# Kernel optimization log

Measured on AMD Instinct MI355X. Metric: run time of the kernel, lower is better.

The kernel has to match this reference:

```python
import jax, jax.numpy as jnp
import numpy as np

K = 3  # deformable kernel size -> K*K = 9 sampling points
EPS = 1e-5


def _bilinear_sample(img, py, px):
    """Bilinear sample img (B,H,W,C) at float pixel coords py,px (B,H,W), zero padding."""
    B, H, W, C = img.shape
    y0f = jnp.floor(py); x0f = jnp.floor(px)
    wy = py - y0f; wx = px - x0f
    y0 = y0f.astype(jnp.int32); x0 = x0f.astype(jnp.int32)
    bidx = jnp.arange(B)[:, None, None]
    out = jnp.zeros(img.shape, img.dtype)
    corners = ((0, 0, (1 - wy) * (1 - wx)), (0, 1, (1 - wy) * wx),
               (1, 0, wy * (1 - wx)), (1, 1, wy * wx))
    for dy, dx, w in corners:
        yy = y0 + dy; xx = x0 + dx
        valid = ((yy >= 0) & (yy < H) & (xx >= 0) & (xx < W)).astype(img.dtype)
        yc = jnp.clip(yy, 0, H - 1); xc = jnp.clip(xx, 0, W - 1)
        out = out + (w * valid)[..., None] * img[bidx, yc, xc]
    return out


def setup_inputs() -> dict:
    key = jax.random.key(0)
    ks = jax.random.split(key, 8)
    B, C, H, W = 8, 256, 64, 64
    return {
        "x1": jax.random.normal(ks[0], (B, C, H, W), jnp.float32),
        "x2": jax.random.normal(ks[1], (B, C, H // 2, W // 2), jnp.float32),
        "dw_w": jax.random.normal(ks[2], (3, 3, 1, C), jnp.float32) * 0.05,
        "dw_b": jnp.zeros((C,), jnp.float32),
        "ln_g": jnp.ones((C,), jnp.float32),
        "ln_b": jnp.zeros((C,), jnp.float32),
        "off_w": jax.random.normal(ks[3], (C, 2 * K * K), jnp.float32) * 0.01,
        "off_b": jnp.zeros((2 * K * K,), jnp.float32),
        "mask_w": jax.random.normal(ks[4], (C, K * K), jnp.float32) * 0.02,
        "mask_b": jnp.zeros((K * K,), jnp.float32),
        "in_w": jax.random.normal(ks[5], (C, C), jnp.float32) * 0.02,
        "in_b": jnp.zeros((C,), jnp.float32),
        "out_w": jax.random.normal(ks[6], (C, C), jnp.float32) * 0.02,
        "out_b": jnp.zeros((C,), jnp.float32),
        "bn_g": jnp.ones((C,), jnp.float32),
        "bn_b": jnp.zeros((C,), jnp.float32),
        "bn_mean": jnp.zeros((C,), jnp.float32),
        "bn_var": jnp.ones((C,), jnp.float32),
    }


def _forward(x1, x2, dw_w, dw_b, ln_g, ln_b, off_w, off_b, mask_w, mask_b,
             in_w, in_b, out_w, out_b, bn_g, bn_b, bn_mean, bn_var):
    B, C, H, W = x1.shape
    # interpolate x2 -> (H,W), bilinear (half-pixel centers, align_corners=False)
    x2r = jax.image.resize(x2, (B, C, H, W), method="linear")
    x21, x22 = jnp.split(x2r, 2, axis=0)
    diff = jnp.abs(x21 - x22)
    guide = jnp.concatenate([diff, diff], axis=0)  # repeat(2,1,1,1)

    v = jnp.transpose(x1, (0, 2, 3, 1))      # (B,H,W,C) values
    f = jnp.transpose(guide, (0, 2, 3, 1))   # (B,H,W,C) guidance

    # DCNv3 input projection
    x_proj = v @ in_w + in_b

    # depthwise 3x3 conv + LayerNorm + GELU on guidance
    feat = jax.lax.conv_general_dilated(
        f, dw_w, (1, 1), "SAME",
        dimension_numbers=("NHWC", "HWIO", "NHWC"),
        feature_group_count=C) + dw_b
    mu = jnp.mean(feat, axis=-1, keepdims=True)
    var = jnp.var(feat, axis=-1, keepdims=True)
    feat = (feat - mu) * jax.lax.rsqrt(var + EPS) * ln_g + ln_b
    feat = jax.nn.gelu(feat)

    offset = (feat @ off_w + off_b).reshape(B, H, W, K * K, 2)  # (..., (dx,dy))
    mask = jax.nn.softmax(feat @ mask_w + mask_b, axis=-1)       # (B,H,W,9)

    base_y = jnp.arange(H, dtype=x1.dtype)[:, None]
    base_x = jnp.arange(W, dtype=x1.dtype)[None, :]
    acc = jnp.zeros((B, H, W, C), x1.dtype)
    for k in range(K * K):
        ky = k // K - 1
        kx = k % K - 1
        py = base_y + ky + offset[..., k, 1]
        px = base_x + kx + offset[..., k, 0]
        acc = acc + mask[..., k:k + 1] * _bilinear_sample(x_proj, py, px)

    y = acc @ out_w + out_b                  # output projection
    y = jnp.transpose(y, (0, 3, 1, 2))       # back to NCHW

    # BatchNorm (inference stats) + ReLU + residual
    scale = bn_g * jax.lax.rsqrt(bn_var + EPS)
    y = y * scale[None, :, None, None] + (bn_b - bn_mean * scale)[None, :, None, None]
    return jax.nn.relu(y) + x1


def reference(x1, x2, dw_w, dw_b, ln_g, ln_b, off_w, off_b, mask_w, mask_b,
              in_w, in_b, out_w, out_b, bn_g, bn_b, bn_mean, bn_var):
    return _forward(x1, x2, dw_w, dw_b, ln_g, ln_b, off_w, off_b, mask_w, mask_b,
                    in_w, in_b, out_w, out_b, bn_g, bn_b, bn_mean, bn_var)
```

## Files before the change

### kernel.cpp

```cpp
#include <hip/hip_runtime.h>
#include <math.h>

#define BB 8
#define CC 256
#define HH 64
#define WW 64
#define H2 32
#define W2 32
#define NPIX (BB*HH*WW)
#define EPSV 1e-5f

typedef unsigned short ushortT;
using short8  = __attribute__((ext_vector_type(8))) short;
using floatx4 = __attribute__((ext_vector_type(4))) float;

__device__ inline float b2f(ushortT u) {
    unsigned int x = ((unsigned int)u) << 16;
    float f; __builtin_memcpy(&f, &x, 4); return f;
}
__device__ inline ushortT f2b(float f) {
    unsigned int x; __builtin_memcpy(&x, &f, 4);
    unsigned int r = x + 0x7fffu + ((x >> 16) & 1u);
    return (ushortT)(r >> 16);
}

__global__ __launch_bounds__(256) void k1_both(const float* __restrict__ x2,
        const float* __restrict__ x1, const float* __restrict__ in_w,
        const float* __restrict__ in_b, const float* __restrict__ out_w,
        const float* __restrict__ off_w, const float* __restrict__ mask_w,
        ushortT* __restrict__ guide, ushortT* __restrict__ x1t,
        ushortT* __restrict__ Bf, float* __restrict__ bwout,
        ushortT* __restrict__ Whf) {
    __shared__ __align__(16) float Xs[2 * 64 * 2 * 33];
    __shared__ __align__(16) ushortT tile[64 * 66];
    int blk0 = blockIdx.x;
    int t = threadIdx.x;

    if (blk0 >= 4353) {
        int s = (blk0 - 4353) * 256 + t;
        int lane = s & 63;
        int kt = (s >> 6) & 7;
        int nt = s >> 9;
        int n = nt * 16 + (lane & 15);
        int k = kt * 32 + (lane >> 4) * 8;
        short8 o;
        #pragma unroll
        for (int j = 0; j < 8; ++j) {
            float wv = 0.f;
            int kk = k + j;
            if (n < 18)      wv = off_w[kk * 18 + n];
            else if (n < 27) wv = mask_w[kk * 9 + (n - 18)];
            o[j] = (short)f2b(wv);
        }
        *(short8*)(Whf + (size_t)s * 8) = o;
        return;
    }
    if (blk0 >= 4096) {
        float* Wl = Xs;
        int j = blk0 - 4096;
        int n = t;
        Wl[n] = (j < CC) ? in_w[(size_t)j * CC + n] : in_b[n];
        __syncthreads();
        float acc = 0.f;
        #pragma unroll 8
        for (int k = 0; k < CC; ++k)
            acc = fmaf(Wl[k], out_w[(size_t)k * CC + n], acc);
        if (j < CC) {
            int lane = (((j >> 3) & 3) << 4) | (n & 15);
            size_t idx = ((size_t)(((n >> 4) * 8 + (j >> 5)) * 64 + lane)) * 8 + (j & 7);
            Bf[idx] = f2b(acc);
        } else {
            bwout[n] = acc;
        }
        return;
    }

    if (blk0 < 2048) {
        int c0 = (blk0 & 3) * 64;
        int y  = (blk0 >> 2) & 63;
        int b  = blk0 >> 8;
        int bb = b & 3;
        float sy = 0.5f * y - 0.25f;
        float fy0 = floorf(sy);
        float wy = sy - fy0;
        int jy0 = (int)fy0;
        int iy0 = max(0, min(H2 - 1, jy0));
        int iy1 = max(0, min(H2 - 1, jy0 + 1));
        #pragma unroll
        for (int i = 0; i < 8; ++i) {
            int e = t + i * 256;
            int q = e >> 10, ch = (e >> 4) & 63, r = (e >> 3) & 1, xg = (e & 7) * 4;
            int iy = r ? iy1 : iy0;
            float4 v = *(const float4*)(x2 +
                (size_t)(((bb + 4 * q) * CC + c0 + ch) * H2 + iy) * W2 + xg);
            float* dst = Xs + (size_t)((q * 64 + ch) * 2 + r) * 33 + xg;
            dst[0] = v.x; dst[1] = v.y; dst[2] = v.z; dst[3] = v.w;
        }
        __syncthreads();
        int x = t & 63, cl = t >> 6;
        float sx = 0.5f * x - 0.25f;
        float fx0 = floorf(sx);
        float wx = sx - fx0;
        int jx0 = (int)fx0;
        int ix0 = max(0, min(W2 - 1, jx0));
        int ix1 = max(0, min(W2 - 1, jx0 + 1));
        float w00 = (1.f - wy) * (1.f - wx), w01 = (1.f - wy) * wx;
        float w10 = wy * (1.f - wx), w11 = wy * wx;
        #pragma unroll
        for (int it = 0; it < 16; ++it) {
            int c = cl + it * 4;
            const float* a  = Xs + (size_t)(c * 2) * 33;
            const float* bq = Xs + (size_t)((64 + c) * 2) * 33;
            float v1 = w00 * a[ix0]  + w01 * a[ix1]  + w10 * a[33 + ix0]  + w11 * a[33 + ix1];
            float v2 = w00 * bq[ix0] + w01 * bq[ix1] + w10 * bq[33 + ix0] + w11 * bq[33 + ix1];
            tile[x * 66 + c] = f2b(fabsf(v1 - v2));
        }
        __syncthreads();
        #pragma unroll
        for (int i = 0; i < 2; ++i) {
            int e = t + i * 256;
            int px = e >> 3, oct = e & 7;
            uint4 o;
            o.x = *(const unsigned int*)(&tile[px * 66 + oct * 8 + 0]);
            o.y = *(const unsigned int*)(&tile[px * 66 + oct * 8 + 2]);
            o.z = *(const unsigned int*)(&tile[px * 66 + oct * 8 + 4]);
            o.w = *(const unsigned int*)(&tile[px * 66 + oct * 8 + 6]);
            *(uint4*)(guide + (size_t)((b * HH + y) * WW + px) * CC + c0 + oct * 8) = o;
        }
    } else {
        int blk = blk0 - 2048;
        int c0 = (blk & 3) * 64;
        int y  = (blk >> 2) & 63;
        int b  = blk >> 8;
        #pragma unroll
        for (int i = 0; i < 4; ++i) {
            int e = t + i * 256;
            int ch = e >> 4, xq = (e & 15) * 4;
            float4 v = *(const float4*)(x1 + (size_t)((b * CC + c0 + ch) * HH + y) * WW + xq);
            tile[(xq + 0) * 66 + ch] = f2b(v.x);
            tile[(xq + 1) * 66 + ch] = f2b(v.y);
            tile[(xq + 2) * 66 + ch] = f2b(v.z);
            tile[(xq + 3) * 66 + ch] = f2b(v.w);
        }
        __syncthreads();
        #pragma unroll
        for (int i = 0; i < 2; ++i) {
            int e = t + i * 256;
            int px = e >> 3, oct = e & 7;
            uint4 o;
            o.x = *(const unsigned int*)(&tile[px * 66 + oct * 8 + 0]);
            o.y = *(const unsigned int*)(&tile[px * 66 + oct * 8 + 2]);
            o.z = *(const unsigned int*)(&tile[px * 66 + oct * 8 + 4]);
            o.w = *(const unsigned int*)(&tile[px * 66 + oct * 8 + 6]);
            *(uint4*)(x1t + (size_t)((b * HH + y) * WW + px) * CC + c0 + oct * 8) = o;
        }
    }
}

__global__ __launch_bounds__(512, 4) void k2ab(const ushortT* __restrict__ guide,
        const float* __restrict__ dw_w, const float* __restrict__ dw_b,
        const float* __restrict__ ln_g, const float* __restrict__ ln_b,
        const ushortT* __restrict__ Whf, const float* __restrict__ off_b,
        const float* __restrict__ mask_b, float* __restrict__ offmask) {
    __shared__ __align__(16) short sfeat[32 * 264];
    __shared__ float O[32 * 36];
    int t = threadIdx.x;
    int blk = ((blockIdx.x & 7) << 7) | (blockIdx.x >> 3);
    int b = blk >> 7, y = (blk >> 1) & 63, xh = (blk & 1) * 32;
    int lane = t & 63, w = t >> 6;
    int cl = lane & 15, rg = lane >> 4;

    {
        int pxl = t >> 4, s = t & 15;
        int c0 = s * 16;
        int xg = xh + pxl;
        float f[16];
        #pragma unroll
        for (int q = 0; q < 4; ++q) {
            float4 d = *(const float4*)(dw_b + c0 + q * 4);
            f[q*4+0]=d.x; f[q*4+1]=d.y; f[q*4+2]=d.z; f[q*4+3]=d.w;
        }
        #pragma unroll
        for (int tap = 0; tap < 9; ++tap) {
            int dy = tap / 3 - 1, dxx = tap % 3 - 1;
            int yy = y + dy, xx = xg + dxx;
            if (yy >= 0 && yy < HH && xx >= 0 && xx < WW) {
                const ushortT* gp = guide + (size_t)((b * HH + yy) * WW + xx) * CC + c0;
                #pragma unroll
                for (int q = 0; q < 2; ++q) {
                    short8 v = *(const short8*)(gp + q * 8);
                    float4 w0 = *(const float4*)(dw_w + tap * CC + c0 + q * 8);
                    float4 w1 = *(const float4*)(dw_w + tap * CC + c0 + q * 8 + 4);
                    float wv[8] = {w0.x, w0.y, w0.z, w0.w, w1.x, w1.y, w1.z, w1.w};
                    #pragma unroll
                    for (int j2 = 0; j2 < 8; ++j2)
                        f[q*8 + j2] = fmaf(b2f((ushortT)v[j2]), wv[j2], f[q*8 + j2]);
                }
            }
        }
        float s1 = 0.f, s2 = 0.f;
        #pragma unroll
        for (int j = 0; j < 16; ++j) { s1 += f[j]; s2 += f[j] * f[j]; }
        #pragma unroll
        for (int off = 8; off; off >>= 1) {
            s1 += __shfl_xor(s1, off);
            s2 += __shfl_xor(s2, off);
        }
        float mean = s1 * (1.0f / CC);
        float var  = s2 * (1.0f / CC) - mean * mean;
        float rs = rsqrtf(var + EPSV);
        #pragma unroll
        for (int q = 0; q < 2; ++q) {
            float4 g0 = *(const float4*)(ln_g + c0 + q * 8);
            float4 g1 = *(const float4*)(ln_g + c0 + q * 8 + 4);
            float4 e0 = *(const float4*)(ln_b + c0 + q * 8);
            float4 e1 = *(const float4*)(ln_b + c0 + q * 8 + 4);
            float gv[8] = {g0.x, g0.y, g0.z, g0.w, g1.x, g1.y, g1.z, g1.w};
            float ev[8] = {e0.x, e0.y, e0.z, e0.w, e1.x, e1.y, e1.z, e1.w};
            short8 sv;
            #pragma unroll
            for (int j2 = 0; j2 < 8; ++j2) {
                float v = (f[q*8 + j2] - mean) * rs * gv[j2] + ev[j2];
                float u2 = 1.5957691216057308f * (v + 0.044715f * v * v * v);
                v = v * __frcp_rn(1.0f + __expf(-u2));
                sv[j2] = (short)f2b(v);
            }
            *(short8*)(&sfeat[pxl * 264 + c0 + q * 8]) = sv;
        }
    }
    __syncthreads();

    if (w < 4) {
        int mt = w >> 1, nt = w & 1;
        floatx4 acc = {0.f, 0.f, 0.f, 0.f};
        #pragma unroll
        for (int kt = 0; kt < 8; ++kt) {
            short8 af  = *(const short8*)(&sfeat[(mt * 16 + cl) * 264 + kt * 32 + rg * 8]);
            short8 bf2 = *(const short8*)(Whf + ((size_t)((nt * 8 + kt) * 64 + lane)) * 8);
            acc = __builtin_amdgcn_mfma_f32_16x16x32_bf16(af, bf2, acc, 0, 0, 0);
        }
        int col = nt * 16 + cl;
        float bias = (col < 18) ? off_b[col] : ((col < 27) ? mask_b[col - 18] : 0.f);
        #pragma unroll
        for (int j = 0; j < 4; ++j) {
            int row = mt * 16 + rg * 4 + j;
            O[row * 36 + col] = acc[j] + bias;
        }
    }
    __syncthreads();

    if (t < 32) {
        float* row = O + t * 36 + 18;
        float mx = row[0];
        #pragma unroll
        for (int k = 1; k < 9; ++k) mx = fmaxf(mx, row[k]);
        float e9[9], ssum = 0.f;
        #pragma unroll
        for (int k = 0; k < 9; ++k) { e9[k] = __expf(row[k] - mx); ssum += e9[k]; }
        float inv = __frcp_rn(ssum);
        #pragma unroll
        for (int k = 0; k < 9; ++k) row[k] = e9[k] * inv;
    }
    __syncthreads();
    #pragma unroll
    for (int i = 0; i < 2; ++i) {
        int idx = t + i * 512;
        int p = idx >> 5, jj = idx & 31;
        offmask[((size_t)blk * 32 + p) * 32 + jj] = O[p * 36 + jj];
    }
}

__global__ __launch_bounds__(512, 4) void k45_fused(const ushortT* __restrict__ x1t,
        const float* __restrict__ offmask, const ushortT* __restrict__ Bf,
        const float* __restrict__ bwout, const float* __restrict__ out_b,
        const float* __restrict__ bn_g, const float* __restrict__ bn_b,
        const float* __restrict__ bn_mean, const float* __restrict__ bn_var,
        const float* __restrict__ x1, float* __restrict__ out) {
    __shared__ __align__(16) char smem[30976];
    short* Asb     = (short*)smem;
    float* s_w     = (float*)(smem + 9216);
    int*   s_idx   = (int*)(smem + 18432);
    float* s_scale = (float*)(smem + 27648);
    float* s_shift = (float*)(smem + 28672);
    float* s_bw    = (float*)(smem + 29696);
    float* s_sum   = (float*)(smem + 30720);
    float* Lo      = (float*)smem;

    int t = threadIdx.x;
    int bm = ((blockIdx.x & 7) << 6) | (blockIdx.x >> 3);
    int m0 = bm * 64;
    int b = bm >> 6, y = bm & 63;
    int lane = t & 63, w = t >> 6;
    int cl = lane & 15, rg = lane >> 4;

    if (t < 256) {
        float scale = bn_g[t] * rsqrtf(bn_var[t] + EPSV);
        s_scale[t] = scale;
        s_shift[t] = out_b[t] * scale + bn_b[t] - bn_mean[t] * scale;
        s_bw[t]    = bwout[t] * scale;
    }
    for (int e = t; e < 576; e += 512) {
        int px = e / 9, k = e - px * 9;
        int p = m0 + px;
        float dxo = offmask[(size_t)p * 32 + 2 * k];
        float dyo = offmask[(size_t)p * 32 + 2 * k + 1];
        float mk  = offmask[(size_t)p * 32 + 18 + k];
        float py  = (float)y  + (float)(k / 3 - 1) + dyo;
        float pxf = (float)px + (float)(k % 3 - 1) + dxo;
        float y0f = floorf(py), x0f = floorf(pxf);
        float wy = py - y0f, wx = pxf - x0f;
        int y0 = (int)y0f, x0 = (int)x0f;
        int y1 = y0 + 1, x1i = x0 + 1;
        float vy0 = (y0 >= 0 && y0 < HH) ? 1.f : 0.f;
        float vy1 = (y1 >= 0 && y1 < HH) ? 1.f : 0.f;
        float vx0 = (x0 >= 0 && x0 < WW) ? 1.f : 0.f;
        float vx1 = (x1i >= 0 && x1i < WW) ? 1.f : 0.f;
        int yc0 = max(0, min(HH - 1, y0)), yc1 = max(0, min(HH - 1, y1));
        int xc0 = max(0, min(WW - 1, x0)), xc1 = max(0, min(WW - 1, x1i));
        int base = b * HH * WW;
        int o = (px * 9 + k) * 4;
        s_idx[o + 0] = (base + yc0 * WW + xc0) * CC;
        s_idx[o + 1] = (base + yc0 * WW + xc1) * CC;
        s_idx[o + 2] = (base + yc1 * WW + xc0) * CC;
        s_idx[o + 3] = (base + yc1 * WW + xc1) * CC;
        s_w[o + 0] = mk * (1.f - wy) * (1.f - wx) * vy0 * vx0;
        s_w[o + 1] = mk * (1.f - wy) * wx * vy0 * vx1;
        s_w[o + 2] = mk * wy * (1.f - wx) * vy1 * vx0;
        s_w[o + 3] = mk * wy * wx * vy1 * vx1;
    }
    __syncthreads();
    if (t < 64) {
        float s = 0.f;
        #pragma unroll
        for (int q = 0; q < 36; ++q) s += s_w[t * 36 + q];
        s_sum[t] = s;
    }
    __syncthreads();

    floatx4 acc[4][2];
    floatx4 zero = {0.f, 0.f, 0.f, 0.f};
    #pragma unroll
    for (int i = 0; i < 4; ++i)
        #pragma unroll
        for (int j = 0; j < 2; ++j) acc[i][j] = zero;

    for (int k0 = 0; k0 < CC; k0 += 64) {
        {
            int px = t >> 3, o8 = t & 7;
            int c = k0 + o8 * 8;
            const float* wp = s_w  + px * 36;
            const int*   ip = s_idx + px * 36;
            float f[8] = {};
            #pragma unroll
            for (int q = 0; q < 36; ++q) {
                float wv = wp[q];
                short8 v = *(const short8*)(x1t + ip[q] + c);
                #pragma unroll
                for (int j = 0; j < 8; ++j)
                    f[j] = fmaf(wv, b2f((ushortT)v[j]), f[j]);
            }
            short8 sv;
            #pragma unroll
            for (int j = 0; j < 8; ++j) sv[j] = (short)f2b(f[j]);
            *(short8*)(&Asb[px * 72 + o8 * 8]) = sv;
        }
        __syncthreads();
        int kt0 = k0 >> 5;
        #pragma unroll
        for (int kk = 0; kk < 2; ++kk) {
            short8 af[4], bfr[2];
            #pragma unroll
            for (int f = 0; f < 4; ++f)
                af[f] = *(const short8*)(&Asb[(f * 16 + cl) * 72 + kk * 32 + rg * 8]);
            #pragma unroll
            for (int fc = 0; fc < 2; ++fc)
                bfr[fc] = *(const short8*)(Bf + ((size_t)((w * 2 + fc) * 8 + kt0 + kk) * 64 + lane) * 8);
            #pragma unroll
            for (int fr = 0; fr < 4; ++fr)
                #pragma unroll
                for (int fc = 0; fc < 2; ++fc)
                    acc[fr][fc] = __builtin_amdgcn_mfma_f32_16x16x32_bf16(
                        af[fr], bfr[fc], acc[fr][fc], 0, 0, 0);
        }
        __syncthreads();
    }

    #pragma unroll
    for (int ph = 0; ph < 4; ++ph) {
        if ((w >> 1) == ph) {
            #pragma unroll
            for (int fc = 0; fc < 2; ++fc) {
                int cloc = (w & 1) * 32 + fc * 16 + cl;
                #pragma unroll
                for (int fr = 0; fr < 4; ++fr) {
                    int mr = fr * 16 + rg * 4;
                    #pragma unroll
                    for (int j = 0; j < 4; ++j)
                        Lo[(mr + j) * 65 + cloc] = acc[fr][fc][j];
                }
            }
        }
        __syncthreads();
        #pragma unroll
        for (int i = 0; i < 8; ++i) {
            int e = t + i * 512;
            int xl = e & 63, cw = e >> 6;
            int co = ph * 64 + cw;
            float val = Lo[xl * 65 + cw] * s_scale[co] + s_sum[xl] * s_bw[co] + s_shift[co];
            val = fmaxf(val, 0.f);
            size_t g = (size_t)((b * CC + co) * HH + y) * WW + xl;
            out[g] = val + x1[g];
        }
        __syncthreads();
    }
}

extern "C" void kernel_launch(void* const* d_in, const int* in_sizes, int n_in,
                              void* d_out, int out_size, void* d_ws, size_t ws_size,
                              hipStream_t stream) {
    const float* x1     = (const float*)d_in[0];
    const float* x2     = (const float*)d_in[1];
    const float* dw_w   = (const float*)d_in[2];
    const float* dw_b   = (const float*)d_in[3];
    const float* ln_g   = (const float*)d_in[4];
    const float* ln_b   = (const float*)d_in[5];
    const float* off_w  = (const float*)d_in[6];
    const float* off_b  = (const float*)d_in[7];
    const float* mask_w = (const float*)d_in[8];
    const float* mask_b = (const float*)d_in[9];
    const float* in_w   = (const float*)d_in[10];
    const float* in_b   = (const float*)d_in[11];
    const float* out_w  = (const float*)d_in[12];
    const float* out_b  = (const float*)d_in[13];
    const float* bn_g   = (const float*)d_in[14];
    const float* bn_b   = (const float*)d_in[15];
    const float* bn_mean= (const float*)d_in[16];
    const float* bn_var = (const float*)d_in[17];
    float* out = (float*)d_out;

    char* wsb = (char*)d_ws;
    const size_t SZ = (size_t)NPIX * CC * 2;
    ushortT* guide   = (ushortT*)wsb;
    ushortT* x1t     = (ushortT*)(wsb + SZ);
    float*   offmask = (float*)(wsb + 2 * SZ);
    float*   bwout   = offmask + (size_t)NPIX * 32;
    ushortT* Bf      = (ushortT*)(bwout + CC);
    ushortT* Whf     = Bf + (size_t)CC * CC;

    hipLaunchKernelGGL(k1_both, dim3(4357), dim3(256), 0, stream, x2, x1, in_w, in_b,
                       out_w, off_w, mask_w, guide, x1t, Bf, bwout, Whf);
    hipLaunchKernelGGL(k2ab,    dim3(1024), dim3(512), 0, stream, guide, dw_w, dw_b,
                       ln_g, ln_b, Whf, off_b, mask_b, offmask);
    hipLaunchKernelGGL(k45_fused, dim3(512), dim3(512), 0, stream, x1t, offmask, Bf,
                       bwout, out_b, bn_g, bn_b, bn_mean, bn_var, x1, out);
}
```

Measured before the change: 98.40 us.

## Double-buffer gathered A tile to overlap bilinear gather with MFMA

The A-operand staging buffer in LDS is now double-buffered. The gather for the next 64-channel chunk is issued before the MFMA work on the current chunk, and one barrier per chunk is removed. The aim is to hide the latency of the scattered global loads behind the matrix math. In exchange, shared memory grows to about 40KB and register pressure rises, which may reduce occupancy under the 512x4 launch bounds.

```diff
diff --git a/kernel.cpp b/kernel.cpp
--- a/kernel.cpp
+++ b/kernel.cpp
@@ -270,20 +270,32 @@
     }
 }
 
+#define GATHER_CHUNK(K0) do {                                            \
+        int c_ = (K0) + o8 * 8;                                          \
+        _Pragma("unroll")                                                \
+        for (int q = 0; q < 36; ++q) {                                   \
+            float wv_ = wp[q];                                           \
+            short8 v_ = *(const short8*)(x1t + ip[q] + c_);              \
+            _Pragma("unroll")                                            \
+            for (int j = 0; j < 8; ++j)                                  \
+                f[j] = fmaf(wv_, b2f((ushortT)v_[j]), f[j]);             \
+        }                                                                \
+    } while (0)
+
 __global__ __launch_bounds__(512, 4) void k45_fused(const ushortT* __restrict__ x1t,
         const float* __restrict__ offmask, const ushortT* __restrict__ Bf,
         const float* __restrict__ bwout, const float* __restrict__ out_b,
         const float* __restrict__ bn_g, const float* __restrict__ bn_b,
         const float* __restrict__ bn_mean, const float* __restrict__ bn_var,
         const float* __restrict__ x1, float* __restrict__ out) {
-    __shared__ __align__(16) char smem[30976];
+    __shared__ __align__(16) char smem[40192];
     short* Asb     = (short*)smem;
-    float* s_w     = (float*)(smem + 9216);
-    int*   s_idx   = (int*)(smem + 18432);
-    float* s_scale = (float*)(smem + 27648);
-    float* s_shift = (float*)(smem + 28672);
-    float* s_bw    = (float*)(smem + 29696);
-    float* s_sum   = (float*)(smem + 30720);
+    float* s_w     = (float*)(smem + 18432);
+    int*   s_idx   = (int*)(smem + 27648);
+    float* s_scale = (float*)(smem + 36864);
+    float* s_shift = (float*)(smem + 37888);
+    float* s_bw    = (float*)(smem + 38912);
+    float* s_sum   = (float*)(smem + 39936);
     float* Lo      = (float*)smem;
 
     int t = threadIdx.x;
@@ -337,6 +349,10 @@
     }
     __syncthreads();
 
+    int px = t >> 3, o8 = t & 7;
+    const float* wp = s_w  + px * 36;
+    const int*   ip = s_idx + px * 36;
+
     floatx4 acc[4][2];
     floatx4 zero = {0.f, 0.f, 0.f, 0.f};
     #pragma unroll
@@ -344,43 +360,47 @@
         #pragma unroll
         for (int j = 0; j < 2; ++j) acc[i][j] = zero;
 
-    for (int k0 = 0; k0 < CC; k0 += 64) {
+    {
+        float f[8] = {};
+        GATHER_CHUNK(0);
+        short8 sv;
+        #pragma unroll
+        for (int j = 0; j < 8; ++j) sv[j] = (short)f2b(f[j]);
+        *(short8*)(&Asb[px * 72 + o8 * 8]) = sv;
+    }
+    __syncthreads();
+
+    #pragma unroll
+    for (int kc = 0; kc < 4; ++kc) {
+        int cur = kc & 1;
+        float f[8] = {};
+        if (kc < 3)
+            GATHER_CHUNK((kc + 1) * 64);
         {
-            int px = t >> 3, o8 = t & 7;
-            int c = k0 + o8 * 8;
-            const float* wp = s_w  + px * 36;
-            const int*   ip = s_idx + px * 36;
-            float f[8] = {};
+            const short* Ab = Asb + cur * 4608;
+            int kt0 = kc * 2;
             #pragma unroll
-            for (int q = 0; q < 36; ++q) {
-                float wv = wp[q];
-                short8 v = *(const short8*)(x1t + ip[q] + c);
+            for (int kk = 0; kk < 2; ++kk) {
+                short8 af[4], bfr[2];
                 #pragma unroll
-                for (int j = 0; j < 8; ++j)
-                    f[j] = fmaf(wv, b2f((ushortT)v[j]), f[j]);
+                for (int fr2 = 0; fr2 < 4; ++fr2)
+                    af[fr2] = *(const short8*)(&Ab[(fr2 * 16 + cl) * 72 + kk * 32 + rg * 8]);
+                #pragma unroll
+                for (int fc = 0; fc < 2; ++fc)
+                    bfr[fc] = *(const short8*)(Bf + ((size_t)((w * 2 + fc) * 8 + kt0 + kk) * 64 + lane) * 8);
+                #pragma unroll
+                for (int fr2 = 0; fr2 < 4; ++fr2)
+                    #pragma unroll
+                    for (int fc = 0; fc < 2; ++fc)
+                        acc[fr2][fc] = __builtin_amdgcn_mfma_f32_16x16x32_bf16(
+                            af[fr2], bfr[fc], acc[fr2][fc], 0, 0, 0);
             }
+        }
+        if (kc < 3) {
             short8 sv;
             #pragma unroll
             for (int j = 0; j < 8; ++j) sv[j] = (short)f2b(f[j]);
-            *(short8*)(&Asb[px * 72 + o8 * 8]) = sv;
-        }
-        __syncthreads();
-        int kt0 = k0 >> 5;
-        #pragma unroll
-        for (int kk = 0; kk < 2; ++kk) {
-            short8 af[4], bfr[2];
-            #pragma unroll
-            for (int f = 0; f < 4; ++f)
-                af[f] = *(const short8*)(&Asb[(f * 16 + cl) * 72 + kk * 32 + rg * 8]);
-            #pragma unroll
-            for (int fc = 0; fc < 2; ++fc)
-                bfr[fc] = *(const short8*)(Bf + ((size_t)((w * 2 + fc) * 8 + kt0 + kk) * 64 + lane) * 8);
-            #pragma unroll
-            for (int fr = 0; fr < 4; ++fr)
-                #pragma unroll
-                for (int fc = 0; fc < 2; ++fc)
-                    acc[fr][fc] = __builtin_amdgcn_mfma_f32_16x16x32_bf16(
-                        af[fr], bfr[fc], acc[fr][fc], 0, 0, 0);
+            *(short8*)(&Asb[(cur ^ 1) * 4608 + px * 72 + o8 * 8]) = sv;
         }
         __syncthreads();
     }
@@ -392,11 +412,11 @@
             for (int fc = 0; fc < 2; ++fc) {
                 int cloc = (w & 1) * 32 + fc * 16 + cl;
                 #pragma unroll
-                for (int fr = 0; fr < 4; ++fr) {
-                    int mr = fr * 16 + rg * 4;
+                for (int fr2 = 0; fr2 < 4; ++fr2) {
+                    int mr = fr2 * 16 + rg * 4;
                     #pragma unroll
                     for (int j = 0; j < 4; ++j)
-                        Lo[(mr + j) * 65 + cloc] = acc[fr][fc][j];
+                        Lo[(mr + j) * 65 + cloc] = acc[fr2][fc][j];
                 }
             }
         }
```

After: 98.07 us. About the same (-0.3%).

## Split fused deformable-gather+GEMM kernel into separate gather and GEMM kernels

Applied to the files above, without the earlier changes.

The fused kernel, which interleaved the bilinear gather with MFMA GEMM tiles under barriers, is split in two. A gather kernel with 4096 blocks of 8 pixels writes the bf16 aggregated features and per-pixel weight sums to workspace, reusing the guide buffer. A separate GEMM kernel with 1024 blocks of 32 pixels loads the full K=256 tile into LDS and runs the MFMA plus the BN/ReLU/residual epilogue. This gives the latency-bound gather more parallelism and removes the per-k-step barriers, at the cost of an extra global round trip for the intermediate and one more launch.

```diff
diff --git a/kernel.cpp b/kernel.cpp
--- a/kernel.cpp
+++ b/kernel.cpp
@@ -270,43 +270,23 @@
     }
 }
 
-__global__ __launch_bounds__(512, 4) void k45_fused(const ushortT* __restrict__ x1t,
-        const float* __restrict__ offmask, const ushortT* __restrict__ Bf,
-        const float* __restrict__ bwout, const float* __restrict__ out_b,
-        const float* __restrict__ bn_g, const float* __restrict__ bn_b,
-        const float* __restrict__ bn_mean, const float* __restrict__ bn_var,
-        const float* __restrict__ x1, float* __restrict__ out) {
-    __shared__ __align__(16) char smem[30976];
-    short* Asb     = (short*)smem;
-    float* s_w     = (float*)(smem + 9216);
-    int*   s_idx   = (int*)(smem + 18432);
-    float* s_scale = (float*)(smem + 27648);
-    float* s_shift = (float*)(smem + 28672);
-    float* s_bw    = (float*)(smem + 29696);
-    float* s_sum   = (float*)(smem + 30720);
-    float* Lo      = (float*)smem;
-
+__global__ __launch_bounds__(256) void kG(const ushortT* __restrict__ x1t,
+        const float* __restrict__ offmask, ushortT* __restrict__ accg,
+        float* __restrict__ sums) {
+    int blk = ((blockIdx.x & 7) << 9) | (blockIdx.x >> 3);
+    int p0 = blk * 8;
     int t = threadIdx.x;
-    int bm = ((blockIdx.x & 7) << 6) | (blockIdx.x >> 3);
-    int m0 = bm * 64;
-    int b = bm >> 6, y = bm & 63;
-    int lane = t & 63, w = t >> 6;
-    int cl = lane & 15, rg = lane >> 4;
-
-    if (t < 256) {
-        float scale = bn_g[t] * rsqrtf(bn_var[t] + EPSV);
-        s_scale[t] = scale;
-        s_shift[t] = out_b[t] * scale + bn_b[t] - bn_mean[t] * scale;
-        s_bw[t]    = bwout[t] * scale;
-    }
-    for (int e = t; e < 576; e += 512) {
-        int px = e / 9, k = e - px * 9;
-        int p = m0 + px;
+    __shared__ int   s_idx[8][9][4];
+    __shared__ float s_w[8][9][4];
+    if (t < 72) {
+        int pxi = t / 9, k = t - pxi * 9;
+        int p = p0 + pxi;
+        int x = p & 63, y = (p >> 6) & 63, b = p >> 12;
         float dxo = offmask[(size_t)p * 32 + 2 * k];
         float dyo = offmask[(size_t)p * 32 + 2 * k + 1];
         float mk  = offmask[(size_t)p * 32 + 18 + k];
-        float py  = (float)y  + (float)(k / 3 - 1) + dyo;
-        float pxf = (float)px + (float)(k % 3 - 1) + dxo;
+        float py  = (float)y + (float)(k / 3 - 1) + dyo;
+        float pxf = (float)x + (float)(k % 3 - 1) + dxo;
         float y0f = floorf(py), x0f = floorf(pxf);
         float wy = py - y0f, wx = pxf - x0f;
         int y0 = (int)y0f, x0 = (int)x0f;
@@ -318,97 +298,127 @@
         int yc0 = max(0, min(HH - 1, y0)), yc1 = max(0, min(HH - 1, y1));
         int xc0 = max(0, min(WW - 1, x0)), xc1 = max(0, min(WW - 1, x1i));
         int base = b * HH * WW;
-        int o = (px * 9 + k) * 4;
-        s_idx[o + 0] = (base + yc0 * WW + xc0) * CC;
-        s_idx[o + 1] = (base + yc0 * WW + xc1) * CC;
-        s_idx[o + 2] = (base + yc1 * WW + xc0) * CC;
-        s_idx[o + 3] = (base + yc1 * WW + xc1) * CC;
-        s_w[o + 0] = mk * (1.f - wy) * (1.f - wx) * vy0 * vx0;
-        s_w[o + 1] = mk * (1.f - wy) * wx * vy0 * vx1;
-        s_w[o + 2] = mk * wy * (1.f - wx) * vy1 * vx0;
-        s_w[o + 3] = mk * wy * wx * vy1 * vx1;
-    }
-    __syncthreads();
-    if (t < 64) {
+        s_idx[pxi][k][0] = (base + yc0 * WW + xc0) * CC;
+        s_idx[pxi][k][1] = (base + yc0 * WW + xc1) * CC;
+        s_idx[pxi][k][2] = (base + yc1 * WW + xc0) * CC;
+        s_idx[pxi][k][3] = (base + yc1 * WW + xc1) * CC;
+        s_w[pxi][k][0] = mk * (1.f - wy) * (1.f - wx) * vy0 * vx0;
+        s_w[pxi][k][1] = mk * (1.f - wy) * wx * vy0 * vx1;
+        s_w[pxi][k][2] = mk * wy * (1.f - wx) * vy1 * vx0;
+        s_w[pxi][k][3] = mk * wy * wx * vy1 * vx1;
+    }
+    __syncthreads();
+    if (t < 8) {
         float s = 0.f;
-        #pragma unroll
-        for (int q = 0; q < 36; ++q) s += s_w[t * 36 + q];
-        s_sum[t] = s;
-    }
-    __syncthreads();
-
-    floatx4 acc[4][2];
+        const float* wq = &s_w[t][0][0];
+        #pragma unroll
+        for (int q = 0; q < 36; ++q) s += wq[q];
+        sums[p0 + t] = s;
+    }
+    int px = t >> 5, cg = t & 31, c0 = cg * 8;
+    const float* wp = &s_w[px][0][0];
+    const int*   ip = &s_idx[px][0][0];
+    float f[8] = {};
+    #pragma unroll
+    for (int q = 0; q < 36; ++q) {
+        float wv = wp[q];
+        short8 v = *(const short8*)(x1t + ip[q] + c0);
+        #pragma unroll
+        for (int j = 0; j < 8; ++j)
+            f[j] = fmaf(wv, b2f((ushortT)v[j]), f[j]);
+    }
+    short8 sv;
+    #pragma unroll
+    for (int j = 0; j < 8; ++j) sv[j] = (short)f2b(f[j]);
+    *(short8*)(accg + (size_t)(p0 + px) * CC + c0) = sv;
+}
+
+__global__ __launch_bounds__(256, 4) void kGEMM(const ushortT* __restrict__ accg,
+        const float* __restrict__ sums, const ushortT* __restrict__ Bf,
+        const float* __restrict__ bwout, const float* __restrict__ out_b,
+        const float* __restrict__ bn_g, const float* __restrict__ bn_b,
+        const float* __restrict__ bn_mean, const float* __restrict__ bn_var,
+        const float* __restrict__ x1, float* __restrict__ out) {
+    __shared__ __align__(16) char smem[20224];
+    short* Asb     = (short*)smem;
+    float* s_scale = (float*)(smem + 16896);
+    float* s_shift = (float*)(smem + 17920);
+    float* s_bw    = (float*)(smem + 18944);
+    float* s_sumL  = (float*)(smem + 19968);
+    float* Lo      = (float*)smem;
+
+    int t = threadIdx.x;
+    int blk = ((blockIdx.x & 7) << 7) | (blockIdx.x >> 3);
+    int m0 = blk * 32;
+    int b = m0 >> 12, y = (m0 >> 6) & 63, xb = m0 & 63;
+    int lane = t & 63, w = t >> 6;
+    int cl = lane & 15, rg = lane >> 4;
+
+    {
+        float scale = bn_g[t] * rsqrtf(bn_var[t] + EPSV);
+        s_scale[t] = scale;
+        s_shift[t] = out_b[t] * scale + bn_b[t] - bn_mean[t] * scale;
+        s_bw[t]    = bwout[t] * scale;
+    }
+    if (t < 32) s_sumL[t] = sums[m0 + t];
+    #pragma unroll
+    for (int i = 0; i < 4; ++i) {
+        int e = t + i * 256;
+        int px = e >> 5, oct = e & 31;
+        *(short8*)(&Asb[px * 264 + oct * 8]) =
+            *(const short8*)(accg + (size_t)(m0 + px) * CC + oct * 8);
+    }
+    __syncthreads();
+
+    floatx4 acc[2][4];
     floatx4 zero = {0.f, 0.f, 0.f, 0.f};
     #pragma unroll
-    for (int i = 0; i < 4; ++i)
-        #pragma unroll
-        for (int j = 0; j < 2; ++j) acc[i][j] = zero;
-
-    for (int k0 = 0; k0 < CC; k0 += 64) {
-        {
-            int px = t >> 3, o8 = t & 7;
-            int c = k0 + o8 * 8;
-            const float* wp = s_w  + px * 36;
-            const int*   ip = s_idx + px * 36;
-            float f[8] = {};
+    for (int i = 0; i < 2; ++i)
+        #pragma unroll
+        for (int j = 0; j < 4; ++j) acc[i][j] = zero;
+
+    #pragma unroll
+    for (int kt = 0; kt < 8; ++kt) {
+        short8 af[2], bfr[4];
+        #pragma unroll
+        for (int f = 0; f < 2; ++f)
+            af[f] = *(const short8*)(&Asb[(f * 16 + cl) * 264 + kt * 32 + rg * 8]);
+        #pragma unroll
+        for (int fc = 0; fc < 4; ++fc)
+            bfr[fc] = *(const short8*)(Bf + ((size_t)((w * 4 + fc) * 8 + kt) * 64 + lane) * 8);
+        #pragma unroll
+        for (int fr = 0; fr < 2; ++fr)
             #pragma unroll
-            for (int q = 0; q < 36; ++q) {
-                float wv = wp[q];
-                short8 v = *(const short8*)(x1t + ip[q] + c);
-                #pragma unroll
-                for (int j = 0; j < 8; ++j)
-                    f[j] = fmaf(wv, b2f((ushortT)v[j]), f[j]);
-            }
-            short8 sv;
-            #pragma unroll
-            for (int j = 0; j < 8; ++j) sv[j] = (short)f2b(f[j]);
-            *(short8*)(&Asb[px * 72 + o8 * 8]) = sv;
-        }
-        __syncthreads();
-        int kt0 = k0 >> 5;
-        #pragma unroll
-        for (int kk = 0; kk < 2; ++kk) {
-            short8 af[4], bfr[2];
-            #pragma unroll
-            for (int f = 0; f < 4; ++f)
-                af[f] = *(const short8*)(&Asb[(f * 16 + cl) * 72 + kk * 32 + rg * 8]);
-            #pragma unroll
-            for (int fc = 0; fc < 2; ++fc)
-                bfr[fc] = *(const short8*)(Bf + ((size_t)((w * 2 + fc) * 8 + kt0 + kk) * 64 + lane) * 8);
-            #pragma unroll
-            for (int fr = 0; fr < 4; ++fr)
-                #pragma unroll
-                for (int fc = 0; fc < 2; ++fc)
-                    acc[fr][fc] = __builtin_amdgcn_mfma_f32_16x16x32_bf16(
-                        af[fr], bfr[fc], acc[fr][fc], 0, 0, 0);
-        }
-        __syncthreads();
-    }
-
-    #pragma unroll
-    for (int ph = 0; ph < 4; ++ph) {
+            for (int fc = 0; fc < 4; ++fc)
+                acc[fr][fc] = __builtin_amdgcn_mfma_f32_16x16x32_bf16(
+                    af[fr], bfr[fc], acc[fr][fc], 0, 0, 0);
+    }
+    __syncthreads();
+
+    #pragma unroll
+    for (int ph = 0; ph < 2; ++ph) {
         if ((w >> 1) == ph) {
             #pragma unroll
-            for (int fc = 0; fc < 2; ++fc) {
-                int cloc = (w & 1) * 32 + fc * 16 + cl;
+            for (int fc = 0; fc < 4; ++fc) {
+                int cloc = (w & 1) * 64 + fc * 16 + cl;
                 #pragma unroll
-                for (int fr = 0; fr < 4; ++fr) {
+                for (int fr = 0; fr < 2; ++fr) {
                     int mr = fr * 16 + rg * 4;
                     #pragma unroll
                     for (int j = 0; j < 4; ++j)
-                        Lo[(mr + j) * 65 + cloc] = acc[fr][fc][j];
+                        Lo[(mr + j) * 129 + cloc] = acc[fr][fc][j];
                 }
             }
         }
         __syncthreads();
         #pragma unroll
-        for (int i = 0; i < 8; ++i) {
-            int e = t + i * 512;
-            int xl = e & 63, cw = e >> 6;
-            int co = ph * 64 + cw;
-            float val = Lo[xl * 65 + cw] * s_scale[co] + s_sum[xl] * s_bw[co] + s_shift[co];
+        for (int i = 0; i < 16; ++i) {
+            int e = t + i * 256;
+            int xl = e & 31, cw = e >> 5;
+            int co = ph * 128 + cw;
+            float val = Lo[xl * 129 + cw] * s_scale[co] + s_sumL[xl] * s_bw[co] + s_shift[co];
             val = fmaxf(val, 0.f);
-            size_t g = (size_t)((b * CC + co) * HH + y) * WW + xl;
+            size_t g = (size_t)((b * CC + co) * HH + y) * WW + xb + xl;
             out[g] = val + x1[g];
         }
         __syncthreads();
@@ -446,11 +456,14 @@
     float*   bwout   = offmask + (size_t)NPIX * 32;
     ushortT* Bf      = (ushortT*)(bwout + CC);
     ushortT* Whf     = Bf + (size_t)CC * CC;
+    float*   sums    = (float*)(Whf + 8192);
+    ushortT* accg    = guide;
 
     hipLaunchKernelGGL(k1_both, dim3(4357), dim3(256), 0, stream, x2, x1, in_w, in_b,
                        out_w, off_w, mask_w, guide, x1t, Bf, bwout, Whf);
     hipLaunchKernelGGL(k2ab,    dim3(1024), dim3(512), 0, stream, guide, dw_w, dw_b,
                        ln_g, ln_b, Whf, off_b, mask_b, offmask);
-    hipLaunchKernelGGL(k45_fused, dim3(512), dim3(512), 0, stream, x1t, offmask, Bf,
+    hipLaunchKernelGGL(kG,      dim3(4096), dim3(256), 0, stream, x1t, offmask, accg, sums);
+    hipLaunchKernelGGL(kGEMM,   dim3(1024), dim3(256), 0, stream, accg, sums, Bf,
                        bwout, out_b, bn_g, bn_b, bn_mean, bn_var, x1, out);
 }
```

Result: slower. 101.6 us (+3.2%).
